# Kernel tuning notes

Hardware: AMD Instinct MI355X
Metric: run time of the kernel (lower is better)

## Reference

```python
import jax, jax.numpy as jnp
import numpy as np

# Spherical-harmonics constants (from _need_const)
A0 = float(np.pi)
A1 = float(2 * np.pi / np.sqrt(3.0))
A2 = float(2 * np.pi / np.sqrt(8.0))
C0 = float(1 / np.sqrt(4 * np.pi))
C1 = float(np.sqrt(3.0) / np.sqrt(4 * np.pi))
C2 = float(3 * np.sqrt(5.0) / np.sqrt(12 * np.pi))
D0 = float(0.5 / np.sqrt(3.0))
# BlendParams defaults (pytorch3d)
SIGMA = 1e-4
GAMMA_B = 1e-4
BG = (1.0, 1.0, 1.0)
ZNEAR, ZFAR, EPS = 1.0, 100.0, 1e-10


def setup_inputs() -> dict:
    key = jax.random.key(0)
    ks = jax.random.split(key, 9)
    N, H, W, K, V, F = 4, 512, 512, 4, 36000, 70000
    texels = jax.random.uniform(ks[0], (N, H, W, K, 3), dtype=jnp.float32)
    b = jax.random.uniform(ks[1], (N, H, W, K, 3), dtype=jnp.float32) + 1e-3
    bary_coords = b / jnp.sum(b, axis=-1, keepdims=True)
    pix_to_face = jax.random.randint(ks[2], (N, H, W, K), -1, F)  # -1 = empty pixel
    zbuf = jax.random.uniform(ks[3], (N, H, W, K), minval=ZNEAR, maxval=ZFAR, dtype=jnp.float32)
    dists = jax.random.normal(ks[4], (N, H, W, K), dtype=jnp.float32) * 1e-4
    verts = jax.random.normal(ks[5], (V, 3), dtype=jnp.float32)
    faces = jax.random.randint(ks[6], (F, 3), 0, V)
    vn = jax.random.normal(ks[7], (V, 3), dtype=jnp.float32)
    vertex_normals = vn / jnp.linalg.norm(vn, axis=-1, keepdims=True)
    gamma = jax.random.normal(ks[8], (N, 27), dtype=jnp.float32) * 0.1
    return dict(texels=texels, bary_coords=bary_coords, zbuf=zbuf, dists=dists,
                verts=verts, vertex_normals=vertex_normals, gamma=gamma,
                pix_to_face=pix_to_face, faces=faces)


def _interp_face_attrs(pix_to_face, bary, attrs):
    # attrs: (F, 3, D); pix_to_face: (N,H,W,K); bary: (N,H,W,K,3)
    mask = (pix_to_face >= 0)
    idx = jnp.where(mask, pix_to_face, 0)
    g = attrs[idx]  # (N,H,W,K,3,D) gather
    out = jnp.einsum('nhwkv,nhwkvd->nhwkd', bary, g)
    return out * mask[..., None].astype(out.dtype)


def reference(texels, bary_coords, zbuf, dists, verts, vertex_normals, gamma, pix_to_face, faces):
    # flip x,y of vertex normals (as in phong_shading)
    vn = vertex_normals * jnp.asarray([-1.0, -1.0, 1.0], vertex_normals.dtype)
    faces_normals = vn[faces]  # (F,3,3)
    pixel_normals = _interp_face_attrs(pix_to_face, bary_coords, faces_normals)  # (N,H,W,K,3)
    # Note: pixel_coords (from verts) is computed in the original but unused since
    # lights/cameras/materials are None -> specular_color = 0.
    g = gamma.reshape(-1, 3, 9)
    g = g.at[:, :, 0].add(0.8)
    g = jnp.transpose(g, (0, 2, 1))  # (N,9,3)
    nx, ny, nz = pixel_normals[..., 0], pixel_normals[..., 1], pixel_normals[..., 2]
    Y = jnp.stack([
        jnp.full_like(nx, A0 * C0),
        -A1 * C1 * ny,
        A1 * C1 * nz,
        -A1 * C1 * nx,
        A2 * C2 * nx * ny,
        -A2 * C2 * ny * nz,
        A2 * C2 * D0 * (3.0 * nz * nz - 1.0),
        -A2 * C2 * nx * nz,
        A2 * C2 * 0.5 * (nx * nx - ny * ny),
    ], axis=-1)  # (N,H,W,K,9)
    lighting = jnp.einsum('nhwki,nij->nhwkj', Y, g)  # (N,H,W,K,3)
    colors = lighting * texels  # specular = 0
    # softmax_rgb_blend (pytorch3d)
    mask = (pix_to_face >= 0).astype(colors.dtype)
    prob = jax.nn.sigmoid(-dists / SIGMA) * mask
    alpha = 1.0 - jnp.prod(1.0 - prob, axis=-1)
    z_inv = (ZFAR - zbuf) / (ZFAR - ZNEAR) * mask
    z_inv_max = jnp.clip(jnp.max(z_inv, axis=-1, keepdims=True), EPS, None)
    w_num = prob * jnp.exp((z_inv - z_inv_max) / GAMMA_B)
    delta = jnp.clip(jnp.exp((EPS - z_inv_max) / GAMMA_B), EPS, None)
    denom = jnp.sum(w_num, axis=-1, keepdims=True) + delta
    weights = w_num / denom  # (N,H,W,K)
    rgb = jnp.einsum('nhwk,nhwkc->nhwc', weights, colors)
    bg = (delta / denom) * jnp.asarray(BG, colors.dtype)  # (N,H,W,3) via broadcast of (N,H,W,1)
    return jnp.concatenate([rgb + bg, alpha[..., None]], axis=-1)  # (N,H,W,4)
```

## Files before the change

kernel.cpp:

```cpp
#include <hip/hip_runtime.h>
#include <math.h>

#define C_A0 3.14159265358979323846f
#define C_A1 3.6275987284684357f
#define C_A2 2.2214414690791831f
#define C_C0 0.28209479177387814f
#define C_C1 0.48860251190291992f
#define C_C2 1.0925484305920792f
#define C_D0 0.28867513459481287f
#define C_SIGMA  1e-4f
#define C_GAMMAB 1e-4f
#define C_ZNEAR  1.0f
#define C_ZFAR   100.0f
#define C_EPS    1e-10f

__global__ __launch_bounds__(256) void build_face_table(
    const int* __restrict__ faces, const float* __restrict__ vn,
    uint4* __restrict__ tbl, int F)
{
    int f = blockIdx.x * 256 + threadIdx.x;
    if (f >= F) return;
    float c[9];
#pragma unroll
    for (int v = 0; v < 3; ++v) {
        int vi = faces[f * 3 + v];
        c[v * 3 + 0] = -vn[vi * 3 + 0];
        c[v * 3 + 1] = -vn[vi * 3 + 1];
        c[v * 3 + 2] =  vn[vi * 3 + 2];
    }
    unsigned long long lo = 0ull, hi = 0ull;
#pragma unroll
    for (int i = 0; i < 9; ++i) {
        int q = (int)rintf(c[i] * 8191.0f);
        q = q < -8191 ? -8191 : (q > 8191 ? 8191 : q);
        unsigned long long u = (unsigned long long)(unsigned)(q + 8192) & 0x3FFFull;
        int b = 14 * i;
        if (b < 64) {
            lo |= u << b;
            if (b > 50) hi |= u >> (64 - b);
        } else {
            hi |= u << (b - 64);
        }
    }
    tbl[f] = make_uint4((unsigned)lo, (unsigned)(lo >> 32),
                        (unsigned)hi, (unsigned)(hi >> 32));
}

__device__ __forceinline__ void unpack9(uint4 q, float* __restrict__ c)
{
    unsigned long long lo = (unsigned long long)q.x | ((unsigned long long)q.y << 32);
    unsigned long long hi = (unsigned long long)q.z | ((unsigned long long)q.w << 32);
#pragma unroll
    for (int i = 0; i < 9; ++i) {
        int b = 14 * i;
        unsigned v;
        if (b <= 50)       v = (unsigned)(lo >> b) & 0x3FFFu;
        else if (b == 56)  v = ((unsigned)(lo >> 56) | ((unsigned)hi << 8)) & 0x3FFFu;
        else               v = (unsigned)(hi >> (b - 64)) & 0x3FFFu;
        c[i] = (float)(int)v * (1.0f / 8191.0f) - (8192.0f / 8191.0f);
    }
}

template <bool USE_TABLE>
__global__ __launch_bounds__(256) void shade_kernel(
    const float* __restrict__ texels,
    const float* __restrict__ bary,
    const float* __restrict__ zbuf,
    const float* __restrict__ dists,
    const float* __restrict__ vn,
    const float* __restrict__ gamma,
    const int*   __restrict__ p2f,
    const int*   __restrict__ faces,
    const uint4* __restrict__ tbl,
    float4* __restrict__ out,
    int npix, int hw)
{
    int pix = blockIdx.x * 256 + threadIdx.x;
    if (pix >= npix) return;
    int n = (blockIdx.x * 256) / hw;
    const float* __restrict__ g = gamma + n * 27;

    int4   f4 = ((const int4*)p2f)[pix];
    int    fidx[4] = { f4.x, f4.y, f4.z, f4.w };

    uint4 qv[4];
#pragma unroll
    for (int k = 0; k < 4; ++k) {
        int fi = fidx[k] >= 0 ? fidx[k] : 0;
        if (USE_TABLE) qv[k] = tbl[fi];
    }

    float4 zb = ((const float4*)zbuf)[pix];
    float4 dd = ((const float4*)dists)[pix];

    float bl[12], tx[12];
    {
        const float4* bp = (const float4*)bary + (size_t)pix * 3;
        float4 b0 = bp[0], b1 = bp[1], b2 = bp[2];
        bl[0]=b0.x; bl[1]=b0.y; bl[2]=b0.z; bl[3]=b0.w;
        bl[4]=b1.x; bl[5]=b1.y; bl[6]=b1.z; bl[7]=b1.w;
        bl[8]=b2.x; bl[9]=b2.y; bl[10]=b2.z; bl[11]=b2.w;
        const float4* tp = (const float4*)texels + (size_t)pix * 3;
        float4 t0 = tp[0], t1 = tp[1], t2 = tp[2];
        tx[0]=t0.x; tx[1]=t0.y; tx[2]=t0.z; tx[3]=t0.w;
        tx[4]=t1.x; tx[5]=t1.y; tx[6]=t1.z; tx[7]=t1.w;
        tx[8]=t2.x; tx[9]=t2.y; tx[10]=t2.z; tx[11]=t2.w;
    }

    float zbv[4]  = { zb.x, zb.y, zb.z, zb.w };
    float ddv[4]  = { dd.x, dd.y, dd.z, dd.w };

    float prob[4], zinv[4], col[4][3];
    float zmax = C_EPS;

#pragma unroll
    for (int k = 0; k < 4; ++k) {
        int fc = fidx[k];
        float m = (fc >= 0) ? 1.0f : 0.0f;
        int fi = (fc >= 0) ? fc : 0;

        float w0 = bl[k * 3 + 0], w1 = bl[k * 3 + 1], w2 = bl[k * 3 + 2];
        float nx, ny, nz;
        if (USE_TABLE) {
            float c[9];
            unpack9(qv[k], c);
            nx = w0 * c[0] + w1 * c[3] + w2 * c[6];
            ny = w0 * c[1] + w1 * c[4] + w2 * c[7];
            nz = w0 * c[2] + w1 * c[5] + w2 * c[8];
        } else {
            nx = 0.0f; ny = 0.0f; nz = 0.0f;
#pragma unroll
            for (int v = 0; v < 3; ++v) {
                int vi = faces[fi * 3 + v];
                float w = bl[k * 3 + v];
                nx += w * (-vn[vi * 3 + 0]);
                ny += w * (-vn[vi * 3 + 1]);
                nz += w * ( vn[vi * 3 + 2]);
            }
        }
        nx *= m; ny *= m; nz *= m;

        float Yv[9];
        Yv[0] = C_A0 * C_C0;
        Yv[1] = -(C_A1 * C_C1) * ny;
        Yv[2] =  (C_A1 * C_C1) * nz;
        Yv[3] = -(C_A1 * C_C1) * nx;
        Yv[4] =  (C_A2 * C_C2) * nx * ny;
        Yv[5] = -(C_A2 * C_C2) * ny * nz;
        Yv[6] =  (C_A2 * C_C2) * C_D0 * (3.0f * nz * nz - 1.0f);
        Yv[7] = -(C_A2 * C_C2) * nx * nz;
        Yv[8] =  (C_A2 * C_C2) * 0.5f * (nx * nx - ny * ny);

#pragma unroll
        for (int c = 0; c < 3; ++c) {
            float l = Yv[0] * (g[c * 9 + 0] + 0.8f);
#pragma unroll
            for (int i = 1; i < 9; ++i) l += Yv[i] * g[c * 9 + i];
            col[k][c] = l * tx[k * 3 + c];
        }

        prob[k] = m / (1.0f + expf(ddv[k] / C_SIGMA));
        zinv[k] = (C_ZFAR - zbv[k]) / (C_ZFAR - C_ZNEAR) * m;
        zmax = fmaxf(zmax, zinv[k]);
    }

    float alpha = 1.0f - (1.0f - prob[0]) * (1.0f - prob[1])
                        * (1.0f - prob[2]) * (1.0f - prob[3]);

    float delta = expf((C_EPS - zmax) / C_GAMMAB);
    delta = fmaxf(delta, C_EPS);

    float wn[4];
    float denom = delta;
#pragma unroll
    for (int k = 0; k < 4; ++k) {
        wn[k] = prob[k] * expf((zinv[k] - zmax) / C_GAMMAB);
        denom += wn[k];
    }
    float inv = 1.0f / denom;

    float r = 0.0f, gc = 0.0f, b = 0.0f;
#pragma unroll
    for (int k = 0; k < 4; ++k) {
        r  += wn[k] * col[k][0];
        gc += wn[k] * col[k][1];
        b  += wn[k] * col[k][2];
    }
    r  = (r  + delta) * inv;
    gc = (gc + delta) * inv;
    b  = (b  + delta) * inv;

    out[pix] = make_float4(r, gc, b, alpha);
}

extern "C" void kernel_launch(void* const* d_in, const int* in_sizes, int n_in,
                              void* d_out, int out_size, void* d_ws, size_t ws_size,
                              hipStream_t stream) {
    const float* texels = (const float*)d_in[0];
    const float* bary   = (const float*)d_in[1];
    const float* zbuf   = (const float*)d_in[2];
    const float* dists  = (const float*)d_in[3];
    const float* vn     = (const float*)d_in[5];
    const float* gamma  = (const float*)d_in[6];
    const int*   p2f    = (const int*)d_in[7];
    const int*   faces  = (const int*)d_in[8];

    int nhwk = in_sizes[2];
    int npix = nhwk / 4;
    int N    = in_sizes[6] / 27;
    int hw   = npix / N;
    int F    = in_sizes[8] / 3;

    float4* out = (float4*)d_out;
    size_t tbl_bytes = (size_t)F * sizeof(uint4);

    int shade_blocks = (npix + 255) / 256;
    if (ws_size >= tbl_bytes) {
        uint4* tbl = (uint4*)d_ws;
        build_face_table<<<(F + 255) / 256, 256, 0, stream>>>(faces, vn, tbl, F);
        shade_kernel<true><<<shade_blocks, 256, 0, stream>>>(
            texels, bary, zbuf, dists, vn, gamma, p2f, faces, tbl, out, npix, hw);
    } else {
        shade_kernel<false><<<shade_blocks, 256, 0, stream>>>(
            texels, bary, zbuf, dists, vn, gamma, p2f, faces, nullptr, out, npix, hw);
    }
}
```

Before: 196.4 us.

## Map one thread per fragment and reduce K via quad shuffles

```diff
diff --git a/kernel.cpp b/kernel.cpp
--- a/kernel.cpp
+++ b/kernel.cpp
@@ -61,6 +61,10 @@
     }
 }
 
+__device__ __forceinline__ float qsum(float v)  { v += __shfl_xor(v, 1); v += __shfl_xor(v, 2); return v; }
+__device__ __forceinline__ float qmax4(float v) { v = fmaxf(v, __shfl_xor(v, 1)); v = fmaxf(v, __shfl_xor(v, 2)); return v; }
+__device__ __forceinline__ float qprod(float v) { v *= __shfl_xor(v, 1); v *= __shfl_xor(v, 2); return v; }
+
 template <bool USE_TABLE>
 __global__ __launch_bounds__(256) void shade_kernel(
     const float* __restrict__ texels,
@@ -73,124 +77,86 @@
     const int*   __restrict__ faces,
     const uint4* __restrict__ tbl,
     float4* __restrict__ out,
-    int npix, int hw)
+    int nfrag, int hwk)
 {
-    int pix = blockIdx.x * 256 + threadIdx.x;
-    if (pix >= npix) return;
-    int n = (blockIdx.x * 256) / hw;
+    int f = blockIdx.x * 256 + threadIdx.x;
+    if (f >= nfrag) return;
+    int n = (blockIdx.x * 256) / hwk;
     const float* __restrict__ g = gamma + n * 27;
 
-    int4   f4 = ((const int4*)p2f)[pix];
-    int    fidx[4] = { f4.x, f4.y, f4.z, f4.w };
+    int fc = p2f[f];
+    int fi = fc >= 0 ? fc : 0;
+    float m = fc >= 0 ? 1.0f : 0.0f;
 
-    uint4 qv[4];
+    uint4 q;
+    if (USE_TABLE) q = tbl[fi];
+
+    float zb = zbuf[f];
+    float dd = dists[f];
+    float w0 = bary[f * 3 + 0], w1 = bary[f * 3 + 1], w2 = bary[f * 3 + 2];
+    float t0 = texels[f * 3 + 0], t1 = texels[f * 3 + 1], t2 = texels[f * 3 + 2];
+
+    float nx, ny, nz;
+    if (USE_TABLE) {
+        float c[9];
+        unpack9(q, c);
+        nx = w0 * c[0] + w1 * c[3] + w2 * c[6];
+        ny = w0 * c[1] + w1 * c[4] + w2 * c[7];
+        nz = w0 * c[2] + w1 * c[5] + w2 * c[8];
+    } else {
+        nx = 0.0f; ny = 0.0f; nz = 0.0f;
+        float wv[3] = { w0, w1, w2 };
 #pragma unroll
-    for (int k = 0; k < 4; ++k) {
-        int fi = fidx[k] >= 0 ? fidx[k] : 0;
-        if (USE_TABLE) qv[k] = tbl[fi];
+        for (int v = 0; v < 3; ++v) {
+            int vi = faces[fi * 3 + v];
+            nx += wv[v] * (-vn[vi * 3 + 0]);
+            ny += wv[v] * (-vn[vi * 3 + 1]);
+            nz += wv[v] * ( vn[vi * 3 + 2]);
+        }
+    }
+    nx *= m; ny *= m; nz *= m;
+
+    float Yv[9];
+    Yv[0] = C_A0 * C_C0;
+    Yv[1] = -(C_A1 * C_C1) * ny;
+    Yv[2] =  (C_A1 * C_C1) * nz;
+    Yv[3] = -(C_A1 * C_C1) * nx;
+    Yv[4] =  (C_A2 * C_C2) * nx * ny;
+    Yv[5] = -(C_A2 * C_C2) * ny * nz;
+    Yv[6] =  (C_A2 * C_C2) * C_D0 * (3.0f * nz * nz - 1.0f);
+    Yv[7] = -(C_A2 * C_C2) * nx * nz;
+    Yv[8] =  (C_A2 * C_C2) * 0.5f * (nx * nx - ny * ny);
+
+    float tex[3] = { t0, t1, t2 };
+    float col[3];
+#pragma unroll
+    for (int c = 0; c < 3; ++c) {
+        float l = Yv[0] * (g[c * 9 + 0] + 0.8f);
+#pragma unroll
+        for (int i = 1; i < 9; ++i) l += Yv[i] * g[c * 9 + i];
+        col[c] = l * tex[c];
     }
 
-    float4 zb = ((const float4*)zbuf)[pix];
-    float4 dd = ((const float4*)dists)[pix];
+    float prob = m / (1.0f + expf(dd / C_SIGMA));
+    float zinv = (C_ZFAR - zb) / (C_ZFAR - C_ZNEAR) * m;
 
-    float bl[12], tx[12];
-    {
-        const float4* bp = (const float4*)bary + (size_t)pix * 3;
-        float4 b0 = bp[0], b1 = bp[1], b2 = bp[2];
-        bl[0]=b0.x; bl[1]=b0.y; bl[2]=b0.z; bl[3]=b0.w;
-        bl[4]=b1.x; bl[5]=b1.y; bl[6]=b1.z; bl[7]=b1.w;
-        bl[8]=b2.x; bl[9]=b2.y; bl[10]=b2.z; bl[11]=b2.w;
-        const float4* tp = (const float4*)texels + (size_t)pix * 3;
-        float4 t0 = tp[0], t1 = tp[1], t2 = tp[2];
-        tx[0]=t0.x; tx[1]=t0.y; tx[2]=t0.z; tx[3]=t0.w;
-        tx[4]=t1.x; tx[5]=t1.y; tx[6]=t1.z; tx[7]=t1.w;
-        tx[8]=t2.x; tx[9]=t2.y; tx[10]=t2.z; tx[11]=t2.w;
+    float zmax = fmaxf(qmax4(zinv), C_EPS);
+    float wn   = prob * expf((zinv - zmax) / C_GAMMAB);
+    float delta = fmaxf(expf((C_EPS - zmax) / C_GAMMAB), C_EPS);
+
+    float denom = qsum(wn) + delta;
+    float r  = qsum(wn * col[0]);
+    float gc = qsum(wn * col[1]);
+    float b  = qsum(wn * col[2]);
+    float alpha = 1.0f - qprod(1.0f - prob);
+
+    if ((threadIdx.x & 3) == 0) {
+        float inv = 1.0f / denom;
+        out[f >> 2] = make_float4((r + delta) * inv,
+                                  (gc + delta) * inv,
+                                  (b + delta) * inv,
+                                  alpha);
     }
-
-    float zbv[4]  = { zb.x, zb.y, zb.z, zb.w };
-    float ddv[4]  = { dd.x, dd.y, dd.z, dd.w };
-
-    float prob[4], zinv[4], col[4][3];
-    float zmax = C_EPS;
-
-#pragma unroll
-    for (int k = 0; k < 4; ++k) {
-        int fc = fidx[k];
-        float m = (fc >= 0) ? 1.0f : 0.0f;
-        int fi = (fc >= 0) ? fc : 0;
-
-        float w0 = bl[k * 3 + 0], w1 = bl[k * 3 + 1], w2 = bl[k * 3 + 2];
-        float nx, ny, nz;
-        if (USE_TABLE) {
-            float c[9];
-            unpack9(qv[k], c);
-            nx = w0 * c[0] + w1 * c[3] + w2 * c[6];
-            ny = w0 * c[1] + w1 * c[4] + w2 * c[7];
-            nz = w0 * c[2] + w1 * c[5] + w2 * c[8];
-        } else {
-            nx = 0.0f; ny = 0.0f; nz = 0.0f;
-#pragma unroll
-            for (int v = 0; v < 3; ++v) {
-                int vi = faces[fi * 3 + v];
-                float w = bl[k * 3 + v];
-                nx += w * (-vn[vi * 3 + 0]);
-                ny += w * (-vn[vi * 3 + 1]);
-                nz += w * ( vn[vi * 3 + 2]);
-            }
-        }
-        nx *= m; ny *= m; nz *= m;
-
-        float Yv[9];
-        Yv[0] = C_A0 * C_C0;
-        Yv[1] = -(C_A1 * C_C1) * ny;
-        Yv[2] =  (C_A1 * C_C1) * nz;
-        Yv[3] = -(C_A1 * C_C1) * nx;
-        Yv[4] =  (C_A2 * C_C2) * nx * ny;
-        Yv[5] = -(C_A2 * C_C2) * ny * nz;
-        Yv[6] =  (C_A2 * C_C2) * C_D0 * (3.0f * nz * nz - 1.0f);
-        Yv[7] = -(C_A2 * C_C2) * nx * nz;
-        Yv[8] =  (C_A2 * C_C2) * 0.5f * (nx * nx - ny * ny);
-
-#pragma unroll
-        for (int c = 0; c < 3; ++c) {
-            float l = Yv[0] * (g[c * 9 + 0] + 0.8f);
-#pragma unroll
-            for (int i = 1; i < 9; ++i) l += Yv[i] * g[c * 9 + i];
-            col[k][c] = l * tx[k * 3 + c];
-        }
-
-        prob[k] = m / (1.0f + expf(ddv[k] / C_SIGMA));
-        zinv[k] = (C_ZFAR - zbv[k]) / (C_ZFAR - C_ZNEAR) * m;
-        zmax = fmaxf(zmax, zinv[k]);
-    }
-
-    float alpha = 1.0f - (1.0f - prob[0]) * (1.0f - prob[1])
-                        * (1.0f - prob[2]) * (1.0f - prob[3]);
-
-    float delta = expf((C_EPS - zmax) / C_GAMMAB);
-    delta = fmaxf(delta, C_EPS);
-
-    float wn[4];
-    float denom = delta;
-#pragma unroll
-    for (int k = 0; k < 4; ++k) {
-        wn[k] = prob[k] * expf((zinv[k] - zmax) / C_GAMMAB);
-        denom += wn[k];
-    }
-    float inv = 1.0f / denom;
-
-    float r = 0.0f, gc = 0.0f, b = 0.0f;
-#pragma unroll
-    for (int k = 0; k < 4; ++k) {
-        r  += wn[k] * col[k][0];
-        gc += wn[k] * col[k][1];
-        b  += wn[k] * col[k][2];
-    }
-    r  = (r  + delta) * inv;
-    gc = (gc + delta) * inv;
-    b  = (b  + delta) * inv;
-
-    out[pix] = make_float4(r, gc, b, alpha);
 }
 
 extern "C" void kernel_launch(void* const* d_in, const int* in_sizes, int n_in,
@@ -205,23 +171,22 @@
     const int*   p2f    = (const int*)d_in[7];
     const int*   faces  = (const int*)d_in[8];
 
-    int nhwk = in_sizes[2];
-    int npix = nhwk / 4;
-    int N    = in_sizes[6] / 27;
-    int hw   = npix / N;
-    int F    = in_sizes[8] / 3;
+    int nfrag = in_sizes[2];
+    int N     = in_sizes[6] / 27;
+    int hwk   = nfrag / N;
+    int F     = in_sizes[8] / 3;
 
     float4* out = (float4*)d_out;
     size_t tbl_bytes = (size_t)F * sizeof(uint4);
 
-    int shade_blocks = (npix + 255) / 256;
+    int shade_blocks = (nfrag + 255) / 256;
     if (ws_size >= tbl_bytes) {
         uint4* tbl = (uint4*)d_ws;
         build_face_table<<<(F + 255) / 256, 256, 0, stream>>>(faces, vn, tbl, F);
         shade_kernel<true><<<shade_blocks, 256, 0, stream>>>(
-            texels, bary, zbuf, dists, vn, gamma, p2f, faces, tbl, out, npix, hw);
+            texels, bary, zbuf, dists, vn, gamma, p2f, faces, tbl, out, nfrag, hwk);
     } else {
         shade_kernel<false><<<shade_blocks, 256, 0, stream>>>(
-            texels, bary, zbuf, dists, vn, gamma, p2f, faces, nullptr, out, npix, hw);
+            texels, bary, zbuf, dists, vn, gamma, p2f, faces, nullptr, out, nfrag, hwk);
     }
 }
```

Result: no change. 195.6 us (-0.4%).
